# Kernel optimization log

Measured on AMD Instinct MI355X. Metric: run time of the kernel, lower is better.

The kernel has to match this reference:

```python
import jax, jax.numpy as jnp
import numpy as np

B, L, D, DEPTH, FF, VOCAB = 2, 2048, 1024, 4, 4096, 32000

def setup_inputs():
    key = jax.random.key(0)
    ks = jax.random.split(key, 16)
    n = lambda k, s, sc: jax.random.normal(k, s, dtype=jnp.float32) * sc
    sw = 0.01 / float(np.sqrt(D))  # xavier_normal with gain 0.01 on square dims
    return dict(
        tokens=jax.random.randint(ks[0], (B, L), 0, VOCAB),
        emb=n(ks[1], (VOCAB, D), 0.02),
        Wz=n(ks[2], (DEPTH, D, D), sw), bz=jnp.zeros((DEPTH, D)),
        Wza=n(ks[3], (DEPTH, D, D), sw), bza=jnp.zeros((DEPTH, D)),
        Wy=n(ks[4], (DEPTH, D, D), sw), by=jnp.zeros((DEPTH, D)),
        Wya=n(ks[5], (DEPTH, D, D), sw), bya=jnp.zeros((DEPTH, D)),
        lc_re=n(ks[6], (DEPTH, D), 1.0), lc_im=n(ks[7], (DEPTH, D), 1.0),
        g_in=jnp.ones((DEPTH, D)), g_sc=jnp.ones((DEPTH, D)), g_ffn=jnp.ones((DEPTH, D)),
        Wf=n(ks[8], (DEPTH, D, FF), 0.02), bf=jnp.zeros((DEPTH, FF)),
        Wfa=n(ks[9], (DEPTH, D, FF), 0.02), bfa=jnp.zeros((DEPTH, FF)),
        Wfo=n(ks[10], (DEPTH, FF, D), 0.02), bfo=jnp.zeros((DEPTH, D)),
        ln_w=jnp.ones((D,)), ln_b=jnp.zeros((D,)),
        Wout=n(ks[11], (D, VOCAB), 0.02), bout=jnp.zeros((VOCAB,)),
    )

def _silu(x):
    return x * jax.nn.sigmoid(x)

def _rms(x, w, eps=1e-6):
    return x * jax.lax.rsqrt(jnp.mean(x * x, axis=-1, keepdims=True) + eps) * w

def reference(tokens, emb, Wz, bz, Wza, bza, Wy, by, Wya, bya, lc_re, lc_im,
              g_in, g_sc, g_ffn, Wf, bf, Wfa, bfa, Wfo, bfo, ln_w, ln_b, Wout, bout):
    Bq, Lq = tokens.shape
    # Embedding with max_norm=1: torch renorms accessed rows to norm <= 1
    e = emb[tokens]
    nrm = jnp.linalg.norm(e, axis=-1, keepdims=True)
    x = e * jnp.minimum(1.0, 1.0 / jnp.maximum(nrm, 1e-7))
    # Decaying phazor kernel (shared across layers; phazor_angle_scale is a fixed buffer)
    angle = jnp.power(0.001, jnp.linspace(0.0, 1.0, D))
    ln_ph = (1e-5 + 1j * angle).astype(jnp.complex64)      # [D]
    t = jnp.arange(Lq, dtype=jnp.float32)
    ph = jnp.exp(t[:, None] * ln_ph[None, :])              # [L, D] complex
    pf = jnp.fft.fft(ph, n=2 * Lq, axis=0)                 # [2L, D]
    decay = jnp.exp(ln_ph)                                 # [D]
    for i in range(DEPTH):
        # --- SConv sublayer (pre-RMSNorm + residual) ---
        xr = x
        xn = _rms(x, g_sc[i])
        z = (xn @ Wz[i] + bz[i]) * _silu(xn @ Wza[i] + bza[i])
        zf = jnp.fft.fft(z.astype(jnp.complex64), n=2 * Lq, axis=1)
        h = jnp.fft.ifft(zf * pf[None], axis=1)[:, :Lq]    # inner-chunk causal decaying conv
        lc = (lc_re[i] + 1j * lc_im[i]).astype(jnp.complex64)
        h = h + lc[None, None, :] * ph[None] * decay[None, None, :]  # cross-chunk state carry
        y = (_rms(h.real, g_in[i]) @ Wy[i] + by[i]) * _silu(xn @ Wya[i] + bya[i])
        x = xr + y
        # --- FFN SwiGLU sublayer (pre-RMSNorm + residual) ---
        xr = x
        xn = _rms(x, g_ffn[i])
        x = xr + ((xn @ Wf[i] + bf[i]) * _silu(xn @ Wfa[i] + bfa[i])) @ Wfo[i] + bfo[i]
    # Final LayerNorm + vocab projection
    mu = jnp.mean(x, axis=-1, keepdims=True)
    var = jnp.mean((x - mu) ** 2, axis=-1, keepdims=True)
    x = (x - mu) * jax.lax.rsqrt(var + 1e-5) * ln_w + ln_b
    return x @ Wout + bout
```

## Files before the change

kernel.cpp:

```cpp
#include <hip/hip_runtime.h>
#include <math.h>

typedef __attribute__((ext_vector_type(8))) short bf16x8;
typedef __attribute__((ext_vector_type(4))) float f32x4;

#define DEVI __device__ __forceinline__

DEVI short f2bf(float f) {
  unsigned u = __builtin_bit_cast(unsigned, f);
  return (short)((u + 0x7fffu + ((u >> 16) & 1u)) >> 16);
}
DEVI float bf2f(short s) {
  unsigned u = ((unsigned)(unsigned short)s) << 16;
  return __builtin_bit_cast(float, u);
}

DEVI float silu_f(float v) { return v / (1.0f + expf(-v)); }

DEVI void async16(const void* g, void* l) {
  __builtin_amdgcn_global_load_lds(
      (const __attribute__((address_space(1))) void*)g,
      (__attribute__((address_space(3))) void*)l, 16, 0, 0);
}

template <int N>
DEVI void waitvm() { asm volatile("s_waitcnt vmcnt(%0)" ::"i"(N) : "memory"); }
DEVI void barrier_mem() { asm volatile("s_barrier" ::: "memory"); }
DEVI void lgkm0_sb() {
  asm volatile("s_waitcnt lgkmcnt(0)" ::: "memory");
  __builtin_amdgcn_sched_barrier(0);
}

template <int NROWT>
DEVI void tile_map(int* bx, int* by) {
  const int nwg = gridDim.x;
  const int lin = blockIdx.x;
  const int q = nwg >> 3;
  const int wgid = (lin & 7) * q + (lin >> 3);
  *by = wgid % NROWT;
  *bx = wgid / NROWT;
}

#define SWZ(r) ((ks ^ (((r) >> 1) & 3)) << 4)

__global__ __launch_bounds__(512, 4) void voc_k(const short* __restrict__ A,
                                                const short* __restrict__ BT,
                                                const float* __restrict__ bias,
                                                float* __restrict__ outp,
                                                int N, int K) {
  __shared__ __align__(16) char lds[3 * 24576];
  int bx, by;
  tile_map<16>(&bx, &by);
  const int row0 = by << 8, col0 = bx << 7;
  const int t = threadIdx.x, w = t >> 6, lane = t & 63;
  const int wm = w >> 1, wn = w & 1;
  const int lr = lane & 15, ks = lane >> 4;
  f32x4 acc[4][4] = {};

  const int sslot = (t & 3) ^ ((t >> 3) & 3);
  const char* gA = (const char*)A + ((size_t)(row0 + (t >> 2)) * K) * 2 + sslot * 16;
  const char* gB = (const char*)BT + ((size_t)(col0 + (t >> 2)) * K) * 2 + sslot * 16;
  const size_t cstep = (size_t)K << 8;
  const int t16 = t << 4;
  const int nkt = K >> 5;

#define SV(nb, kt)                                                            \
  {                                                                           \
    const size_t co = (size_t)(kt) << 6;                                      \
    async16(gA + co, (nb) + t16);                                             \
    async16(gA + cstep + co, (nb) + 8192 + t16);                              \
    async16(gB + co, (nb) + 16384 + t16);                                     \
  }

  SV(lds, 0);
  SV(lds + 24576, 1);

  for (int kt = 0; kt < nkt; ++kt) {
    const char* base = lds + (kt % 3) * 24576;
    char* nb = lds + ((kt + 2) % 3) * 24576;
    if (kt + 1 < nkt) waitvm<3>();
    else waitvm<0>();
    barrier_mem();
    if (kt + 2 < nkt) SV(nb, kt + 2);
    bf16x8 af[4], bfr[4];
#pragma unroll
    for (int m = 0; m < 4; ++m) {
      const int r = (wm << 6) + (m << 4) + lr;
      af[m] = *(const bf16x8*)(base + r * 64 + SWZ(r));
    }
#pragma unroll
    for (int n = 0; n < 4; ++n) {
      const int rb = (wn << 6) + (n << 4) + lr;
      bfr[n] = *(const bf16x8*)(base + 16384 + rb * 64 + SWZ(rb));
    }
    lgkm0_sb();
    __builtin_amdgcn_s_setprio(1);
#pragma unroll
    for (int m = 0; m < 4; ++m)
#pragma unroll
      for (int n = 0; n < 4; ++n)
        acc[m][n] = __builtin_amdgcn_mfma_f32_16x16x32_bf16(af[m], bfr[n], acc[m][n], 0, 0, 0);
    __builtin_amdgcn_s_setprio(0);
    __builtin_amdgcn_sched_barrier(0);
  }

  const int orow = row0 + (wm << 6) + (ks << 2);
  const int ocol = col0 + (wn << 6) + lr;
#pragma unroll
  for (int m = 0; m < 4; ++m) {
#pragma unroll
    for (int n = 0; n < 4; ++n) {
      const int c = ocol + (n << 4);
      const float bv = bias[c];
#pragma unroll
      for (int i = 0; i < 4; ++i) {
        const int r = orow + (m << 4) + i;
        outp[(size_t)r * N + c] = acc[m][n][i] + bv;
      }
    }
  }
#undef SV
}

__global__ __launch_bounds__(256, 2) void dual_k(const short* __restrict__ A,
                                                 const short* __restrict__ BT1,
                                                 const short* __restrict__ BT2,
                                                 const float* __restrict__ bias1,
                                                 const float* __restrict__ bias2,
                                                 short* __restrict__ outp,
                                                 int N, int K) {
  __shared__ __align__(16) char lds[3 * 24576];
  int bx, by;
  tile_map<32>(&bx, &by);
  const int row0 = by << 7, col0 = bx << 7;
  const int t = threadIdx.x, w = t >> 6, lane = t & 63;
  const int wm = w >> 1, wn = w & 1;
  const int lr = lane & 15, ks = lane >> 4;
  f32x4 acc1[4][4] = {}, acc2[4][4] = {};

  const int sslot = (t & 3) ^ ((t >> 3) & 3);
  const char* gA = (const char*)A + ((size_t)(row0 + (t >> 2)) * K) * 2 + sslot * 16;
  const char* gB1 = (const char*)BT1 + ((size_t)(col0 + (t >> 2)) * K) * 2 + sslot * 16;
  const char* gB2 = (const char*)BT2 + ((size_t)(col0 + (t >> 2)) * K) * 2 + sslot * 16;
  const size_t cstep = (size_t)K << 7;
  const int t16 = t << 4;
  const int nkt = K >> 5;

#define SD(nb, kt)                                                            \
  {                                                                           \
    const size_t co = (size_t)(kt) << 6;                                      \
    async16(gA + co, (nb) + t16);                                             \
    async16(gA + cstep + co, (nb) + 4096 + t16);                              \
    async16(gB1 + co, (nb) + 8192 + t16);                                     \
    async16(gB1 + cstep + co, (nb) + 12288 + t16);                            \
    async16(gB2 + co, (nb) + 16384 + t16);                                    \
    async16(gB2 + cstep + co, (nb) + 20480 + t16);                            \
  }

  SD(lds, 0);
  SD(lds + 24576, 1);

  for (int kt = 0; kt < nkt; ++kt) {
    const char* base = lds + (kt % 3) * 24576;
    char* nb = lds + ((kt + 2) % 3) * 24576;
    if (kt + 1 < nkt) waitvm<6>();
    else waitvm<0>();
    barrier_mem();
    if (kt + 2 < nkt) SD(nb, kt + 2);
    bf16x8 af[4], b1r[4], b2r[4];
#pragma unroll
    for (int m = 0; m < 4; ++m) {
      const int r = (wm << 6) + (m << 4) + lr;
      af[m] = *(const bf16x8*)(base + r * 64 + SWZ(r));
    }
#pragma unroll
    for (int n = 0; n < 4; ++n) {
      const int rb = (wn << 6) + (n << 4) + lr;
      b1r[n] = *(const bf16x8*)(base + 8192 + rb * 64 + SWZ(rb));
      b2r[n] = *(const bf16x8*)(base + 16384 + rb * 64 + SWZ(rb));
    }
    lgkm0_sb();
    __builtin_amdgcn_s_setprio(1);
#pragma unroll
    for (int m = 0; m < 4; ++m)
#pragma unroll
      for (int n = 0; n < 4; ++n) {
        acc1[m][n] = __builtin_amdgcn_mfma_f32_16x16x32_bf16(af[m], b1r[n], acc1[m][n], 0, 0, 0);
        acc2[m][n] = __builtin_amdgcn_mfma_f32_16x16x32_bf16(af[m], b2r[n], acc2[m][n], 0, 0, 0);
      }
    __builtin_amdgcn_s_setprio(0);
    __builtin_amdgcn_sched_barrier(0);
  }

  const int orow = row0 + (wm << 6) + (ks << 2);
  const int ocol = col0 + (wn << 6) + lr;
#pragma unroll
  for (int m = 0; m < 4; ++m) {
#pragma unroll
    for (int n = 0; n < 4; ++n) {
      const int c = ocol + (n << 4);
      const float bv1 = bias1[c], bv2 = bias2[c];
#pragma unroll
      for (int i = 0; i < 4; ++i) {
        const int r = orow + (m << 4) + i;
        outp[(size_t)r * N + c] = f2bf((acc1[m][n][i] + bv1) * silu_f(acc2[m][n][i] + bv2));
      }
    }
  }
#undef SD
}

__global__ __launch_bounds__(256, 2) void triple_k(const short* __restrict__ A,
                                                   const short* __restrict__ BT1,
                                                   const short* __restrict__ BT2,
                                                   const short* __restrict__ BT3,
                                                   const float* __restrict__ b1,
                                                   const float* __restrict__ b2,
                                                   const float* __restrict__ b3,
                                                   short* __restrict__ zout,
                                                   short* __restrict__ yaout,
                                                   int N, int K) {
  constexpr int PBB = 28672;
  __shared__ __align__(16) char lds[2 * PBB];
  int bx, by;
  tile_map<64>(&bx, &by);
  const int row0 = by << 6, col0 = bx << 7;
  const int t = threadIdx.x, w = t >> 6, lane = t & 63;
  const int wr = w >> 1, wc = w & 1;
  const int lr = lane & 15, ks = lane >> 4;
  f32x4 acc1[2][4] = {}, acc2[2][4] = {}, acc3[2][4] = {};

  const int sslot = (t & 3) ^ ((t >> 3) & 3);
  const char* gA = (const char*)A + ((size_t)(row0 + (t >> 2)) * K) * 2 + sslot * 16;
  const size_t brow = ((size_t)(col0 + (t >> 2)) * K) * 2 + sslot * 16;
  const char* gB1 = (const char*)BT1 + brow;
  const char* gB2 = (const char*)BT2 + brow;
  const char* gB3 = (const char*)BT3 + brow;
  const size_t cstep = (size_t)K * 128;
  const int t16 = t << 4;
  const int nkt = K >> 5;

#define STA(nb, kt) async16(gA + (size_t)(kt) * 64, (nb) + t16)
#define STB(nb, kt, gp, off)                                                  \
  {                                                                           \
    const size_t co = (size_t)(kt) * 64;                                      \
    async16((gp) + co, (nb) + (off) + t16);                                   \
    async16((gp) + cstep + co, (nb) + (off) + 4096 + t16);                    \
  }

  { char* nb = lds; STA(nb, 0); STB(nb, 0, gB1, 4096); STB(nb, 0, gB2, 12288); STB(nb, 0, gB3, 20480); }

  for (int kt = 0; kt < nkt; ++kt) {
    const int ktn = kt + 1;
    const char* base = lds + (kt & 1) * PBB;
    char* nb = lds + (ktn & 1) * PBB;
    bf16x8 af[2], bfr[4];
    waitvm<4>();
    barrier_mem();
    if (ktn < nkt) { STA(nb, ktn); STB(nb, ktn, gB1, 4096); }
#pragma unroll
    for (int m = 0; m < 2; ++m) {
      const int r = (wr << 5) + (m << 4) + lr;
      af[m] = *(const bf16x8*)(base + r * 64 + SWZ(r));
    }
#pragma unroll
    for (int n = 0; n < 4; ++n) {
      const int rb = (wc << 6) + (n << 4) + lr;
      bfr[n] = *(const bf16x8*)(base + 4096 + rb * 64 + SWZ(rb));
    }
    lgkm0_sb();
    __builtin_amdgcn_s_setprio(1);
#pragma unroll
    for (int m = 0; m < 2; ++m)
#pragma unroll
      for (int n = 0; n < 4; ++n)
        acc1[m][n] = __builtin_amdgcn_mfma_f32_16x16x32_bf16(af[m], bfr[n], acc1[m][n], 0, 0, 0);
    __builtin_amdgcn_s_setprio(0);
    __builtin_amdgcn_sched_barrier(0);
    if (ktn < nkt) waitvm<5>();
    else waitvm<2>();
    barrier_mem();
    if (ktn < nkt) STB(nb, ktn, gB2, 12288);
#pragma unroll
    for (int n = 0; n < 4; ++n) {
      const int rb = (wc << 6) + (n << 4) + lr;
      bfr[n] = *(const bf16x8*)(base + 12288 + rb * 64 + SWZ(rb));
    }
    lgkm0_sb();
    __builtin_amdgcn_s_setprio(1);
#pragma unroll
    for (int m = 0; m < 2; ++m)
#pragma unroll
      for (int n = 0; n < 4; ++n)
        acc2[m][n] = __builtin_amdgcn_mfma_f32_16x16x32_bf16(af[m], bfr[n], acc2[m][n], 0, 0, 0);
    __builtin_amdgcn_s_setprio(0);
    __builtin_amdgcn_sched_barrier(0);
    if (ktn < nkt) waitvm<5>();
    else waitvm<0>();
    barrier_mem();
    if (ktn < nkt) STB(nb, ktn, gB3, 20480);
#pragma unroll
    for (int n = 0; n < 4; ++n) {
      const int rb = (wc << 6) + (n << 4) + lr;
      bfr[n] = *(const bf16x8*)(base + 20480 + rb * 64 + SWZ(rb));
    }
    lgkm0_sb();
    __builtin_amdgcn_s_setprio(1);
#pragma unroll
    for (int m = 0; m < 2; ++m)
#pragma unroll
      for (int n = 0; n < 4; ++n)
        acc3[m][n] = __builtin_amdgcn_mfma_f32_16x16x32_bf16(af[m], bfr[n], acc3[m][n], 0, 0, 0);
    __builtin_amdgcn_s_setprio(0);
    __builtin_amdgcn_sched_barrier(0);
  }

  const int orow = row0 + (wr << 5) + (ks << 2);
  const int ocol = col0 + (wc << 6) + lr;
#pragma unroll
  for (int m = 0; m < 2; ++m) {
#pragma unroll
    for (int n = 0; n < 4; ++n) {
      const int c = ocol + (n << 4);
      const float bv1 = b1[c], bv2 = b2[c], bv3 = b3[c];
#pragma unroll
      for (int i = 0; i < 4; ++i) {
        const int r = orow + (m << 4) + i;
        const size_t idx = (size_t)r * N + c;
        zout[idx] = f2bf((acc1[m][n][i] + bv1) * silu_f(acc2[m][n][i] + bv2));
        yaout[idx] = f2bf(acc3[m][n][i] + bv3);
      }
    }
  }
#undef STA
#undef STB
}

template <int MODE, int BM, int BN, int WM, int WN, int NBUF>
__global__ __launch_bounds__(256, 2) void gemm_k(const short* __restrict__ A,
                                                 const short* __restrict__ BT,
                                                 const float* __restrict__ bias,
                                                 const short* __restrict__ aux,
                                                 void* __restrict__ outp,
                                                 int N, int K) {
  constexpr int MF = WM / 16, NF = WN / 16;
  constexpr int NWN = BN / WN;
  constexpr int PBB = (BM + BN) * 64;
  constexpr int DEPTH = NBUF - 1;
  constexpr int L = (BM + BN) / 64;
  static_assert((BM / WM) * (BN / WN) == 4, "4 waves");
  __shared__ __align__(16) char lds[NBUF * PBB];
  int bx, by;
  tile_map<4096 / BM>(&bx, &by);
  const int row0 = by * BM, col0 = bx * BN;
  const int t = threadIdx.x, w = t >> 6, lane = t & 63;
  const int wr = w / NWN, wc = w % NWN;
  f32x4 acc[MF][NF] = {};

  const int sslot = (t & 3) ^ ((t >> 3) & 3);
  const char* gA0 = (const char*)A + ((size_t)(row0 + (t >> 2)) * K) * 2 + sslot * 16;
  const char* gB0 = (const char*)BT + ((size_t)(col0 + (t >> 2)) * K) * 2 + sslot * 16;
  const size_t ccstep = (size_t)K * 128;
  const int wb = w << 10;
  const int lr = lane & 15, ks = lane >> 4;

  const int NIT = K >> 5;
  auto stage = [&](int buf, int it) {
    char* dst = lds + buf * PBB;
    const size_t io = (size_t)it * 64;
#pragma unroll
    for (int cc = 0; cc < BM / 64; ++cc)
      async16(gA0 + io + cc * ccstep, dst + cc * 4096 + wb);
#pragma unroll
    for (int cc = 0; cc < BN / 64; ++cc)
      async16(gB0 + io + cc * ccstep, dst + BM * 64 + cc * 4096 + wb);
  };

#pragma unroll
  for (int pit = 0; pit < DEPTH; ++pit) stage(pit, pit);

  for (int it = 0; it < NIT; ++it) {
    const int rem = NIT - it;
    if (rem >= DEPTH + 1) waitvm<L * (DEPTH - 1)>();
    else if (rem >= 2) waitvm<L>();
    else waitvm<0>();
    barrier_mem();
    if (it + DEPTH < NIT) stage((it + DEPTH) % NBUF, it + DEPTH);
    const char* base = lds + (it % NBUF) * PBB;
    bf16x8 af[MF], bfr[NF];
#pragma unroll
    for (int m = 0; m < MF; ++m) {
      const int r = wr * WM + m * 16 + lr;
      af[m] = *(const bf16x8*)(base + r * 64 + SWZ(r));
    }
#pragma unroll
    for (int n = 0; n < NF; ++n) {
      const int r = wc * WN + n * 16 + lr;
      bfr[n] = *(const bf16x8*)(base + BM * 64 + r * 64 + SWZ(r));
    }
    lgkm0_sb();
    __builtin_amdgcn_s_setprio(1);
#pragma unroll
    for (int m = 0; m < MF; ++m)
#pragma unroll
      for (int n = 0; n < NF; ++n)
        acc[m][n] = __builtin_amdgcn_mfma_f32_16x16x32_bf16(af[m], bfr[n], acc[m][n], 0, 0, 0);
    __builtin_amdgcn_s_setprio(0);
    __builtin_amdgcn_sched_barrier(0);
  }

  const int orow = row0 + wr * WM + (ks << 2);
  const int ocol = col0 + wc * WN + lr;
#pragma unroll
  for (int m = 0; m < MF; ++m) {
#pragma unroll
    for (int n = 0; n < NF; ++n) {
      const int c = ocol + (n << 4);
      const float bv = bias[c];
#pragma unroll
      for (int i = 0; i < 4; ++i) {
        const int r = orow + (m << 4) + i;
        const size_t idx = (size_t)r * N + c;
        float v = acc[m][n][i] + bv;
        if (MODE == 0) ((float*)outp)[idx] = v;
        else if (MODE == 3) ((float*)outp)[idx] += v * silu_f(bf2f(aux[idx]));
        else ((float*)outp)[idx] += v;
      }
    }
  }
}

__global__ __launch_bounds__(256) void transp_k(const float* __restrict__ W,
                                                short* __restrict__ WT,
                                                int R, int C) {
  __shared__ float tile[32][33];
  const size_t moff = (size_t)blockIdx.z * R * C;
  const float* Wp = W + moff;
  short* Tp = WT + moff;
  const int c0 = blockIdx.x << 5, r0 = blockIdx.y << 5;
  const int tx = threadIdx.x, ty = threadIdx.y;
#pragma unroll
  for (int i = 0; i < 4; ++i)
    tile[ty + 8 * i][tx] = Wp[(size_t)(r0 + ty + 8 * i) * C + (c0 + tx)];
  __syncthreads();
#pragma unroll
  for (int i = 0; i < 4; ++i)
    Tp[(size_t)(c0 + ty + 8 * i) * R + (r0 + tx)] = f2bf(tile[tx][ty + 8 * i]);
}

__global__ __launch_bounds__(256) void embed_k(const int* __restrict__ tok,
                                               const float* __restrict__ emb,
                                               float* __restrict__ x) {
  const int row = blockIdx.x, t = threadIdx.x, w = t >> 6, lane = t & 63;
  const int token = tok[row];
  float4 v = ((const float4*)(emb + (size_t)token * 1024))[t];
  float ss = v.x * v.x + v.y * v.y + v.z * v.z + v.w * v.w;
#pragma unroll
  for (int off = 32; off; off >>= 1) ss += __shfl_xor(ss, off, 64);
  __shared__ float red[4];
  if (lane == 0) red[w] = ss;
  __syncthreads();
  const float nrm = sqrtf(red[0] + red[1] + red[2] + red[3]);
  const float sc = fminf(1.0f, 1.0f / fmaxf(nrm, 1e-7f));
  v.x *= sc; v.y *= sc; v.z *= sc; v.w *= sc;
  ((float4*)(x + (size_t)row * 1024))[t] = v;
}

template <int BF>
__global__ __launch_bounds__(256) void rms_k(const void* __restrict__ xin,
                                             const float* __restrict__ g,
                                             short* __restrict__ o) {
  const int row = blockIdx.x, t = threadIdx.x, w = t >> 6, lane = t & 63;
  float v0, v1, v2, v3;
  if (BF) {
    short4 s = ((const short4*)((const short*)xin + (size_t)row * 1024))[t];
    v0 = bf2f(s.x); v1 = bf2f(s.y); v2 = bf2f(s.z); v3 = bf2f(s.w);
  } else {
    float4 v = ((const float4*)((const float*)xin + (size_t)row * 1024))[t];
    v0 = v.x; v1 = v.y; v2 = v.z; v3 = v.w;
  }
  float ss = v0 * v0 + v1 * v1 + v2 * v2 + v3 * v3;
#pragma unroll
  for (int off = 32; off; off >>= 1) ss += __shfl_xor(ss, off, 64);
  __shared__ float red[4];
  if (lane == 0) red[w] = ss;
  __syncthreads();
  const float sc = rsqrtf((red[0] + red[1] + red[2] + red[3]) * (1.0f / 1024.0f) + 1e-6f);
  float4 gv = ((const float4*)g)[t];
  short4 ov = make_short4(f2bf(v0 * sc * gv.x), f2bf(v1 * sc * gv.y),
                          f2bf(v2 * sc * gv.z), f2bf(v3 * sc * gv.w));
  *(short4*)(o + (size_t)row * 1024 + 4 * t) = ov;
}

__global__ __launch_bounds__(256) void ln_k(const float* __restrict__ x,
                                            const float* __restrict__ lw,
                                            const float* __restrict__ lb,
                                            short* __restrict__ o) {
  const int row = blockIdx.x, t = threadIdx.x, w = t >> 6, lane = t & 63;
  float4 v = ((const float4*)(x + (size_t)row * 1024))[t];
  float s1 = v.x + v.y + v.z + v.w;
  float s2 = v.x * v.x + v.y * v.y + v.z * v.z + v.w * v.w;
#pragma unroll
  for (int off = 32; off; off >>= 1) {
    s1 += __shfl_xor(s1, off, 64);
    s2 += __shfl_xor(s2, off, 64);
  }
  __shared__ float red[8];
  if (lane == 0) { red[w] = s1; red[4 + w] = s2; }
  __syncthreads();
  const float mu = (red[0] + red[1] + red[2] + red[3]) * (1.0f / 1024.0f);
  const float ex2 = (red[4] + red[5] + red[6] + red[7]) * (1.0f / 1024.0f);
  const float rs = rsqrtf(ex2 - mu * mu + 1e-5f);
  float4 wv = ((const float4*)lw)[t];
  float4 bv = ((const float4*)lb)[t];
  short4 ov = make_short4(f2bf((v.x - mu) * rs * wv.x + bv.x),
                          f2bf((v.y - mu) * rs * wv.y + bv.y),
                          f2bf((v.z - mu) * rs * wv.z + bv.z),
                          f2bf((v.w - mu) * rs * wv.w + bv.w));
  *(short4*)(o + (size_t)row * 1024 + 4 * t) = ov;
}

DEVI void decay_of(int d, float* dr, float* di) {
  const float ang = powf(1e-3f, (float)d * (1.0f / 1023.0f));
  float sn, cs;
  sincosf(ang, &sn, &cs);
  const float mag = expf(1e-5f);
  *dr = mag * cs; *di = mag * sn;
}

__global__ __launch_bounds__(256) void s1_k(const short* __restrict__ z,
                                            float* __restrict__ Er, float* __restrict__ Ei) {
  const int d = (blockIdx.x << 8) + threadIdx.x;
  const int c = blockIdx.y, b = blockIdx.z;
  float dr, di;
  decay_of(d, &dr, &di);
  const short* zp = z + ((size_t)(b * 2048 + c * 64) << 10) + d;
  float sr = 0.0f, si = 0.0f;
  for (int k = 0; k < 64; ++k) {
    float zv = bf2f(zp[(size_t)k << 10]);
    float nr = dr * sr - di * si + zv;
    si = dr * si + di * sr;
    sr = nr;
  }
  const int idx = ((b << 5) + c) * 1024 + d;
  Er[idx] = sr; Ei[idx] = si;
}

__global__ __launch_bounds__(256) void s3_k(const short* __restrict__ z,
                                            const float* __restrict__ Er,
                                            const float* __restrict__ Ei,
                                            const float* __restrict__ lcre,
                                            const float* __restrict__ lcim,
                                            short* __restrict__ h) {
  const int d = (blockIdx.x << 8) + threadIdx.x;
  const int c = blockIdx.y, b = blockIdx.z;
  float dr, di;
  decay_of(d, &dr, &di);
  float ar = dr, ai = di;
#pragma unroll
  for (int q = 0; q < 6; ++q) { float nr = ar * ar - ai * ai; ai = 2.0f * ar * ai; ar = nr; }
  float sr = 0.0f, si = 0.0f;
  for (int cc = 0; cc < c; ++cc) {
    const int eidx = ((b << 5) + cc) * 1024 + d;
    const float er = Er[eidx], ei = Ei[eidx];
    const float nr = ar * sr - ai * si + er;
    si = ar * si + ai * sr + ei;
    sr = nr;
  }
  float wr = 1.0f, wi = 0.0f, br = ar, bi = ai;
  int e = c;
  while (e) {
    if (e & 1) { float nr = wr * br - wi * bi; wi = wr * bi + wi * br; wr = nr; }
    float nb = br * br - bi * bi; bi = 2.0f * br * bi; br = nb;
    e >>= 1;
  }
  { float nr = wr * dr - wi * di; wi = wr * di + wi * dr; wr = nr; }
  const float lr_ = lcre[d], li_ = lcim[d];
  const size_t base = ((size_t)(b * 2048 + c * 64) << 10) + d;
  for (int k = 0; k < 64; ++k) {
    const float zv = bf2f(z[base + ((size_t)k << 10)]);
    const float nr = dr * sr - di * si + zv;
    si = dr * si + di * sr;
    sr = nr;
    h[base + ((size_t)k << 10)] = f2bf(sr + lr_ * wr - li_ * wi);
    const float nw = wr * dr - wi * di;
    wi = wr * di + wi * dr;
    wr = nw;
  }
}

extern "C" void kernel_launch(void* const* d_in, const int* in_sizes, int n_in,
                              void* d_out, int out_size, void* d_ws, size_t ws_size,
                              hipStream_t stream) {
  const int* tokens = (const int*)d_in[0];
  const float* emb = (const float*)d_in[1];
  const float* Wz = (const float*)d_in[2];
  const float* bz = (const float*)d_in[3];
  const float* Wza = (const float*)d_in[4];
  const float* bza = (const float*)d_in[5];
  const float* Wy = (const float*)d_in[6];
  const float* by = (const float*)d_in[7];
  const float* Wya = (const float*)d_in[8];
  const float* bya = (const float*)d_in[9];
  const float* lc_re = (const float*)d_in[10];
  const float* lc_im = (const float*)d_in[11];
  const float* g_in = (const float*)d_in[12];
  const float* g_sc = (const float*)d_in[13];
  const float* g_ffn = (const float*)d_in[14];
  const float* Wf = (const float*)d_in[15];
  const float* bf = (const float*)d_in[16];
  const float* Wfa = (const float*)d_in[17];
  const float* bfa = (const float*)d_in[18];
  const float* Wfo = (const float*)d_in[19];
  const float* bfo = (const float*)d_in[20];
  const float* ln_w = (const float*)d_in[21];
  const float* ln_b = (const float*)d_in[22];
  const float* Wout = (const float*)d_in[23];
  const float* bout = (const float*)d_in[24];

  char* p = (char*)d_ws;
  float* xb = (float*)p;   p += (size_t)4096 * 1024 * 4;
  short* zb = (short*)p;   p += (size_t)4096 * 1024 * 2;
  short* hb = (short*)p;   p += (size_t)4096 * 1024 * 2;
  short* yab = (short*)p;  p += (size_t)4096 * 1024 * 2;
  float* Er = (float*)p;   p += (size_t)2 * 32 * 1024 * 4;
  float* Ei = (float*)p;   p += (size_t)2 * 32 * 1024 * 4;
  short* xnb = (short*)p;  p += (size_t)4096 * 1024 * 2;
  short* hnb = (short*)p;  p += (size_t)4096 * 1024 * 2;
  short* gb = (short*)p;   p += (size_t)4096 * 4096 * 2;
  short* WzT = (short*)p;  p += (size_t)4 * 1024 * 1024 * 2;
  short* WzaT = (short*)p; p += (size_t)4 * 1024 * 1024 * 2;
  short* WyT = (short*)p;  p += (size_t)4 * 1024 * 1024 * 2;
  short* WyaT = (short*)p; p += (size_t)4 * 1024 * 1024 * 2;
  short* WfT = (short*)p;  p += (size_t)4 * 1024 * 4096 * 2;
  short* WfaT = (short*)p; p += (size_t)4 * 1024 * 4096 * 2;
  short* WfoT = (short*)p; p += (size_t)4 * 1024 * 4096 * 2;
  short* WoutT = (short*)p; p += (size_t)32000 * 1024 * 2;

  const dim3 tb(32, 8);
  transp_k<<<dim3(32, 32, 4), tb, 0, stream>>>(Wz, WzT, 1024, 1024);
  transp_k<<<dim3(32, 32, 4), tb, 0, stream>>>(Wza, WzaT, 1024, 1024);
  transp_k<<<dim3(32, 32, 4), tb, 0, stream>>>(Wy, WyT, 1024, 1024);
  transp_k<<<dim3(32, 32, 4), tb, 0, stream>>>(Wya, WyaT, 1024, 1024);
  transp_k<<<dim3(128, 32, 4), tb, 0, stream>>>(Wf, WfT, 1024, 4096);
  transp_k<<<dim3(128, 32, 4), tb, 0, stream>>>(Wfa, WfaT, 1024, 4096);
  transp_k<<<dim3(32, 128, 4), tb, 0, stream>>>(Wfo, WfoT, 4096, 1024);
  transp_k<<<dim3(1000, 32, 1), tb, 0, stream>>>(Wout, WoutT, 1024, 32000);

  embed_k<<<4096, 256, 0, stream>>>(tokens, emb, xb);

  for (int i = 0; i < 4; ++i) {
    const size_t dd = (size_t)i * 1024 * 1024;
    const size_t dv = (size_t)i * 1024;
    const size_t dw = (size_t)i * 1024 * 4096;
    const size_t df = (size_t)i * 4096;
    rms_k<0><<<4096, 256, 0, stream>>>(xb, g_sc + dv, xnb);
    triple_k<<<512, 256, 0, stream>>>(xnb, WzT + dd, WzaT + dd, WyaT + dd,
                                      bz + dv, bza + dv, bya + dv, zb, yab, 1024, 1024);
    s1_k<<<dim3(4, 32, 2), 256, 0, stream>>>(zb, Er, Ei);
    s3_k<<<dim3(4, 32, 2), 256, 0, stream>>>(zb, Er, Ei, lc_re + dv, lc_im + dv, hb);
    rms_k<1><<<4096, 256, 0, stream>>>(hb, g_in + dv, hnb);
    gemm_k<3, 64, 128, 32, 64, 3><<<512, 256, 0, stream>>>(
        hnb, WyT + dd, by + dv, yab, xb, 1024, 1024);
    rms_k<0><<<4096, 256, 0, stream>>>(xb, g_ffn + dv, xnb);
    dual_k<<<1024, 256, 0, stream>>>(xnb, WfT + dw, WfaT + dw, bf + df, bfa + df,
                                     gb, 4096, 1024);
    gemm_k<4, 64, 128, 32, 64, 4><<<512, 256, 0, stream>>>(
        gb, WfoT + dw, bfo + dv, nullptr, xb, 1024, 4096);
  }

  ln_k<<<4096, 256, 0, stream>>>(xb, ln_w, ln_b, xnb);
  voc_k<<<4000, 512, 0, stream>>>(xnb, WoutT, bout, (float*)d_out, 32000, 1024);

  (void)in_sizes; (void)n_in; (void)out_size; (void)ws_size;
}
```

Measured before the change: 1.592 ms.

## Rework vocab and FFN dual GEMM tiling, warp layout and LDS pipeline

The vocab projection kernel drops from 8 to 4 waves per block. Each wave now computes a 128x64 sub-tile with 8x4 accumulators, using a double-buffered LDS ring with an extra barrier before refilling the buffer just read. The FFN gate/up dual GEMM becomes an 8-wave, 256x128-tile kernel with a 4-stage LDS ring, and it processes the two weight matrices in sequential phases that share one B-fragment register set. The aim is more data reuse per block and lower register pressure, at the cost of occupancy, extra barriers and a shallower vocab pipeline.

```diff
diff --git a/kernel.cpp b/kernel.cpp
--- a/kernel.cpp
+++ b/kernel.cpp
@@ -43,24 +43,24 @@
 
 #define SWZ(r) ((ks ^ (((r) >> 1) & 3)) << 4)
 
-__global__ __launch_bounds__(512, 4) void voc_k(const short* __restrict__ A,
+__global__ __launch_bounds__(256, 2) void voc_k(const short* __restrict__ A,
                                                 const short* __restrict__ BT,
                                                 const float* __restrict__ bias,
                                                 float* __restrict__ outp,
                                                 int N, int K) {
-  __shared__ __align__(16) char lds[3 * 24576];
+  __shared__ __align__(16) char lds[2 * 24576];
   int bx, by;
   tile_map<16>(&bx, &by);
   const int row0 = by << 8, col0 = bx << 7;
   const int t = threadIdx.x, w = t >> 6, lane = t & 63;
   const int wm = w >> 1, wn = w & 1;
   const int lr = lane & 15, ks = lane >> 4;
-  f32x4 acc[4][4] = {};
+  f32x4 acc[8][4] = {};
 
   const int sslot = (t & 3) ^ ((t >> 3) & 3);
   const char* gA = (const char*)A + ((size_t)(row0 + (t >> 2)) * K) * 2 + sslot * 16;
   const char* gB = (const char*)BT + ((size_t)(col0 + (t >> 2)) * K) * 2 + sslot * 16;
-  const size_t cstep = (size_t)K << 8;
+  const size_t cstep = (size_t)K << 7;
   const int t16 = t << 4;
   const int nkt = K >> 5;
 
@@ -68,35 +68,38 @@
   {                                                                           \
     const size_t co = (size_t)(kt) << 6;                                      \
     async16(gA + co, (nb) + t16);                                             \
-    async16(gA + cstep + co, (nb) + 8192 + t16);                              \
+    async16(gA + cstep + co, (nb) + 4096 + t16);                              \
+    async16(gA + 2 * cstep + co, (nb) + 8192 + t16);                          \
+    async16(gA + 3 * cstep + co, (nb) + 12288 + t16);                         \
     async16(gB + co, (nb) + 16384 + t16);                                     \
+    async16(gB + cstep + co, (nb) + 20480 + t16);                             \
   }
 
   SV(lds, 0);
   SV(lds + 24576, 1);
 
   for (int kt = 0; kt < nkt; ++kt) {
-    const char* base = lds + (kt % 3) * 24576;
-    char* nb = lds + ((kt + 2) % 3) * 24576;
-    if (kt + 1 < nkt) waitvm<3>();
+    char* buf = lds + (kt & 1) * 24576;
+    if (kt + 1 < nkt) waitvm<6>();
     else waitvm<0>();
     barrier_mem();
-    if (kt + 2 < nkt) SV(nb, kt + 2);
-    bf16x8 af[4], bfr[4];
-#pragma unroll
-    for (int m = 0; m < 4; ++m) {
-      const int r = (wm << 6) + (m << 4) + lr;
-      af[m] = *(const bf16x8*)(base + r * 64 + SWZ(r));
+    bf16x8 af[8], bfr[4];
+#pragma unroll
+    for (int m = 0; m < 8; ++m) {
+      const int r = (wm << 7) + (m << 4) + lr;
+      af[m] = *(const bf16x8*)(buf + r * 64 + SWZ(r));
     }
 #pragma unroll
     for (int n = 0; n < 4; ++n) {
       const int rb = (wn << 6) + (n << 4) + lr;
-      bfr[n] = *(const bf16x8*)(base + 16384 + rb * 64 + SWZ(rb));
+      bfr[n] = *(const bf16x8*)(buf + 16384 + rb * 64 + SWZ(rb));
     }
     lgkm0_sb();
+    barrier_mem();
+    if (kt + 2 < nkt) SV(buf, kt + 2);
     __builtin_amdgcn_s_setprio(1);
 #pragma unroll
-    for (int m = 0; m < 4; ++m)
+    for (int m = 0; m < 8; ++m)
 #pragma unroll
       for (int n = 0; n < 4; ++n)
         acc[m][n] = __builtin_amdgcn_mfma_f32_16x16x32_bf16(af[m], bfr[n], acc[m][n], 0, 0, 0);
@@ -104,10 +107,10 @@
     __builtin_amdgcn_sched_barrier(0);
   }
 
-  const int orow = row0 + (wm << 6) + (ks << 2);
+  const int orow = row0 + (wm << 7) + (ks << 2);
   const int ocol = col0 + (wn << 6) + lr;
 #pragma unroll
-  for (int m = 0; m < 4; ++m) {
+  for (int m = 0; m < 8; ++m) {
 #pragma unroll
     for (int n = 0; n < 4; ++n) {
       const int c = ocol + (n << 4);
@@ -122,17 +125,17 @@
 #undef SV
 }
 
-__global__ __launch_bounds__(256, 2) void dual_k(const short* __restrict__ A,
-                                                 const short* __restrict__ BT1,
-                                                 const short* __restrict__ BT2,
-                                                 const float* __restrict__ bias1,
-                                                 const float* __restrict__ bias2,
-                                                 short* __restrict__ outp,
-                                                 int N, int K) {
-  __shared__ __align__(16) char lds[3 * 24576];
+__global__ __launch_bounds__(512, 1) void dual8_k(const short* __restrict__ A,
+                                                  const short* __restrict__ BT1,
+                                                  const short* __restrict__ BT2,
+                                                  const float* __restrict__ bias1,
+                                                  const float* __restrict__ bias2,
+                                                  short* __restrict__ outp,
+                                                  int N, int K) {
+  __shared__ __align__(16) char lds[4 * 32768];
   int bx, by;
-  tile_map<32>(&bx, &by);
-  const int row0 = by << 7, col0 = bx << 7;
+  tile_map<16>(&bx, &by);
+  const int row0 = by << 8, col0 = bx << 7;
   const int t = threadIdx.x, w = t >> 6, lane = t & 63;
   const int wm = w >> 1, wn = w & 1;
   const int lr = lane & 15, ks = lane >> 4;
@@ -142,52 +145,66 @@
   const char* gA = (const char*)A + ((size_t)(row0 + (t >> 2)) * K) * 2 + sslot * 16;
   const char* gB1 = (const char*)BT1 + ((size_t)(col0 + (t >> 2)) * K) * 2 + sslot * 16;
   const char* gB2 = (const char*)BT2 + ((size_t)(col0 + (t >> 2)) * K) * 2 + sslot * 16;
-  const size_t cstep = (size_t)K << 7;
+  const size_t cstep = (size_t)K << 8;
   const int t16 = t << 4;
   const int nkt = K >> 5;
 
-#define SD(nb, kt)                                                            \
+#define SAD(nb, kt)                                                           \
   {                                                                           \
     const size_t co = (size_t)(kt) << 6;                                      \
     async16(gA + co, (nb) + t16);                                             \
-    async16(gA + cstep + co, (nb) + 4096 + t16);                              \
-    async16(gB1 + co, (nb) + 8192 + t16);                                     \
-    async16(gB1 + cstep + co, (nb) + 12288 + t16);                            \
-    async16(gB2 + co, (nb) + 16384 + t16);                                    \
-    async16(gB2 + cstep + co, (nb) + 20480 + t16);                            \
-  }
-
-  SD(lds, 0);
-  SD(lds + 24576, 1);
+    async16(gA + cstep + co, (nb) + 8192 + t16);                              \
+  }
+#define SB1D(nb, kt) async16(gB1 + ((size_t)(kt) << 6), (nb) + 16384 + t16)
+#define SB2D(nb, kt) async16(gB2 + ((size_t)(kt) << 6), (nb) + 24576 + t16)
+
+  SAD(lds, 0); SB1D(lds, 0); SB2D(lds, 0);
+  SAD(lds + 32768, 1); SB1D(lds + 32768, 1); SB2D(lds + 32768, 1);
+  SAD(lds + 65536, 2); SB1D(lds + 65536, 2); SB2D(lds + 65536, 2);
 
   for (int kt = 0; kt < nkt; ++kt) {
-    const char* base = lds + (kt % 3) * 24576;
-    char* nb = lds + ((kt + 2) % 3) * 24576;
-    if (kt + 1 < nkt) waitvm<6>();
+    const char* base = lds + (kt & 3) * 32768;
+    char* nb = lds + ((kt + 3) & 3) * 32768;
+    const int rem = nkt - kt;
+    bf16x8 af[4], bfr[4];
+    if (rem > 2) waitvm<8>();
+    else if (rem == 2) waitvm<4>();
     else waitvm<0>();
     barrier_mem();
-    if (kt + 2 < nkt) SD(nb, kt + 2);
-    bf16x8 af[4], b1r[4], b2r[4];
+    if (kt + 3 < nkt) SAD(nb, kt + 3);
+#pragma unroll
+    for (int n = 0; n < 4; ++n) {
+      const int rb = (wn << 6) + (n << 4) + lr;
+      bfr[n] = *(const bf16x8*)(base + 16384 + rb * 64 + SWZ(rb));
+    }
 #pragma unroll
     for (int m = 0; m < 4; ++m) {
       const int r = (wm << 6) + (m << 4) + lr;
       af[m] = *(const bf16x8*)(base + r * 64 + SWZ(r));
     }
-#pragma unroll
-    for (int n = 0; n < 4; ++n) {
-      const int rb = (wn << 6) + (n << 4) + lr;
-      b1r[n] = *(const bf16x8*)(base + 8192 + rb * 64 + SWZ(rb));
-      b2r[n] = *(const bf16x8*)(base + 16384 + rb * 64 + SWZ(rb));
-    }
     lgkm0_sb();
     __builtin_amdgcn_s_setprio(1);
 #pragma unroll
     for (int m = 0; m < 4; ++m)
 #pragma unroll
-      for (int n = 0; n < 4; ++n) {
-        acc1[m][n] = __builtin_amdgcn_mfma_f32_16x16x32_bf16(af[m], b1r[n], acc1[m][n], 0, 0, 0);
-        acc2[m][n] = __builtin_amdgcn_mfma_f32_16x16x32_bf16(af[m], b2r[n], acc2[m][n], 0, 0, 0);
-      }
+      for (int n = 0; n < 4; ++n)
+        acc1[m][n] = __builtin_amdgcn_mfma_f32_16x16x32_bf16(af[m], bfr[n], acc1[m][n], 0, 0, 0);
+    __builtin_amdgcn_s_setprio(0);
+    __builtin_amdgcn_sched_barrier(0);
+    barrier_mem();
+    if (kt + 3 < nkt) { SB1D(nb, kt + 3); SB2D(nb, kt + 3); }
+#pragma unroll
+    for (int n = 0; n < 4; ++n) {
+      const int rb = (wn << 6) + (n << 4) + lr;
+      bfr[n] = *(const bf16x8*)(base + 24576 + rb * 64 + SWZ(rb));
+    }
+    lgkm0_sb();
+    __builtin_amdgcn_s_setprio(1);
+#pragma unroll
+    for (int m = 0; m < 4; ++m)
+#pragma unroll
+      for (int n = 0; n < 4; ++n)
+        acc2[m][n] = __builtin_amdgcn_mfma_f32_16x16x32_bf16(af[m], bfr[n], acc2[m][n], 0, 0, 0);
     __builtin_amdgcn_s_setprio(0);
     __builtin_amdgcn_sched_barrier(0);
   }
@@ -207,7 +224,9 @@
       }
     }
   }
-#undef SD
+#undef SAD
+#undef SB1D
+#undef SB2D
 }
 
 __global__ __launch_bounds__(256, 2) void triple_k(const short* __restrict__ A,
@@ -663,14 +682,14 @@
     gemm_k<3, 64, 128, 32, 64, 3><<<512, 256, 0, stream>>>(
         hnb, WyT + dd, by + dv, yab, xb, 1024, 1024);
     rms_k<0><<<4096, 256, 0, stream>>>(xb, g_ffn + dv, xnb);
-    dual_k<<<1024, 256, 0, stream>>>(xnb, WfT + dw, WfaT + dw, bf + df, bfa + df,
+    dual8_k<<<512, 512, 0, stream>>>(xnb, WfT + dw, WfaT + dw, bf + df, bfa + df,
                                      gb, 4096, 1024);
     gemm_k<4, 64, 128, 32, 64, 4><<<512, 256, 0, stream>>>(
         gb, WfoT + dw, bfo + dv, nullptr, xb, 1024, 4096);
   }
 
   ln_k<<<4096, 256, 0, stream>>>(xb, ln_w, ln_b, xnb);
-  voc_k<<<4000, 512, 0, stream>>>(xnb, WoutT, bout, (float*)d_out, 32000, 1024);
+  voc_k<<<4000, 256, 0, stream>>>(xnb, WoutT, bout, (float*)d_out, 32000, 1024);
 
   (void)in_sizes; (void)n_in; (void)out_size; (void)ws_size;
 }
```

Result: no change. 1.566 ms (-1.7%).
